# Kernel optimization log

Hardware: AMD Instinct MI355X
Metric: run time of the kernel (lower is better)

Reference implementation:

```python
import jax, jax.numpy as jnp
import numpy as np

N_NODES = 50000


def _sage_conv(x, src, dst, W_l, W_r, b, num_nodes):
    # message = x[src]; scatter-mean onto dst (PyG SAGEConv aggr='mean')
    msg = x[src]                                                # [E, C_in]
    agg_sum = jax.ops.segment_sum(msg, dst, num_segments=num_nodes)
    deg = jax.ops.segment_sum(jnp.ones((src.shape[0],), x.dtype), dst,
                              num_segments=num_nodes)
    agg = agg_sum / jnp.maximum(deg, 1.0)[:, None]              # mean, deg clamped to 1
    # lin_l(agg) + lin_r(x); bias lives in lin_l (PyG default)
    return agg @ W_l.T + x @ W_r.T + b


def setup_inputs() -> dict:
    key = jax.random.key(0)
    ks = jax.random.split(key, 8)
    C = 128
    s = 1.0 / np.sqrt(C)
    x = jax.random.normal(ks[0], (N_NODES, C), dtype=jnp.float32)
    edge_index = jax.random.randint(ks[1], (2, 800000), 0, N_NODES, dtype=jnp.int64)
    W1_l = jax.random.uniform(ks[2], (C, C), jnp.float32, -s, s)
    W1_r = jax.random.uniform(ks[3], (C, C), jnp.float32, -s, s)
    b1 = jax.random.uniform(ks[4], (C,), jnp.float32, -s, s)
    W2_l = jax.random.uniform(ks[5], (C, C), jnp.float32, -s, s)
    W2_r = jax.random.uniform(ks[6], (C, C), jnp.float32, -s, s)
    b2 = jax.random.uniform(ks[7], (C,), jnp.float32, -s, s)
    return {"x": x, "edge_index": edge_index,
            "W1_l": W1_l, "W1_r": W1_r, "b1": b1,
            "W2_l": W2_l, "W2_r": W2_r, "b2": b2}


def reference(x, edge_index, W1_l, W1_r, b1, W2_l, W2_r, b2):
    src, dst = edge_index[0], edge_index[1]
    h = _sage_conv(x, src, dst, W1_l, W1_r, b1, N_NODES)
    h = jax.nn.relu(h)  # dropout p=0.0 -> no-op
    out = _sage_conv(h, src, dst, W2_l, W2_r, b2, N_NODES)
    return out
```

## Files before the change

### kernel.cpp

```cpp
#include <hip/hip_runtime.h>

#define NCH 128
#define MAXBKT 512
#define BKT_SHIFT 7
#define BKT_NODES 128
#define BIN_BATCH 4096
#define NHIST 128

typedef __attribute__((ext_vector_type(8))) short bf16x8;
typedef __attribute__((ext_vector_type(4))) float f32x4;

__device__ __forceinline__ unsigned short f2bf_rne(float f) {
  unsigned u = __float_as_uint(f);
  unsigned r = u + 0x7FFF + ((u >> 16) & 1);
  return (unsigned short)(r >> 16);
}

__global__ __launch_bounds__(256) void k_bkthist(const int* __restrict__ dst,
                                                 int* __restrict__ partial,
                                                 int nE, int nBkt) {
  __shared__ int h[MAXBKT];
  int t = threadIdx.x;
  h[t] = 0; h[t + 256] = 0;
  __syncthreads();
  for (int e = blockIdx.x * 256 + t; e < nE; e += gridDim.x * 256)
    atomicAdd(&h[dst[e] >> BKT_SHIFT], 1);
  __syncthreads();
  partial[blockIdx.x * MAXBKT + t] = h[t];
  partial[blockIdx.x * MAXBKT + t + 256] = h[t + 256];
}

__global__ __launch_bounds__(512) void k_bktscan(const int* __restrict__ partial,
                                                 int* __restrict__ bktBase,
                                                 int* __restrict__ bktCursor, int nBkt) {
  __shared__ int sc[512];
  int t = threadIdx.x;
  int v = 0;
#pragma unroll 8
  for (int b = 0; b < NHIST; b++) v += partial[b * MAXBKT + t];
  sc[t] = v;
  __syncthreads();
  for (int off = 1; off < 512; off <<= 1) {
    int u = (t >= off) ? sc[t - off] : 0;
    __syncthreads();
    sc[t] += u;
    __syncthreads();
  }
  bktBase[t] = sc[t] - v;
  if (t == 511) bktBase[512] = sc[511];
  bktCursor[t] = 0;
}

__global__ __launch_bounds__(256) void k_bin(const int* __restrict__ src,
                                             const int* __restrict__ dst,
                                             const int* __restrict__ bktBase,
                                             int* __restrict__ bktCursor,
                                             uint2* __restrict__ binned,
                                             int nE, int nBkt) {
  __shared__ int hist[MAXBKT];
  __shared__ int boff[MAXBKT];
  int t = threadIdx.x;
  hist[t] = 0; hist[t + 256] = 0;
  __syncthreads();

  int eb = blockIdx.x * BIN_BATCH;
  uint2 pr[16];
  int rk[16];
#pragma unroll
  for (int i = 0; i < 16; i++) {
    int e = eb + t + i * 256;
    if (e < nE) {
      pr[i] = make_uint2((unsigned)src[e], (unsigned)dst[e]);
      rk[i] = atomicAdd(&hist[pr[i].y >> BKT_SHIFT], 1);
    } else rk[i] = -1;
  }
  __syncthreads();
  for (int i = t; i < nBkt; i += 256)
    boff[i] = hist[i] ? atomicAdd(&bktCursor[i], hist[i]) : 0;
  __syncthreads();
#pragma unroll
  for (int i = 0; i < 16; i++) {
    if (rk[i] >= 0) {
      int b = pr[i].y >> BKT_SHIFT;
      binned[bktBase[b] + boff[b] + rk[i]] = pr[i];
    }
  }
}

__global__ __launch_bounds__(256) void k_build(const uint2* __restrict__ binned,
                                               const int* __restrict__ bktBase,
                                               int* __restrict__ start,
                                               float* __restrict__ invdeg,
                                               int* __restrict__ srcSorted,
                                               int nN, int nE) {
  __shared__ int cnt[BKT_NODES];
  __shared__ int sc[BKT_NODES];
  __shared__ int cur[BKT_NODES];
  int b = blockIdx.x, t = threadIdx.x;
  int base = b << BKT_SHIFT;
  int e0 = bktBase[b], e1 = bktBase[b + 1];

  if (t < BKT_NODES) { cnt[t] = 0; cur[t] = 0; }
  __syncthreads();
  for (int i = e0 + t; i < e1; i += 256)
    atomicAdd(&cnt[binned[i].y - base], 1);
  __syncthreads();
  if (t < BKT_NODES) sc[t] = cnt[t];
  __syncthreads();
  for (int off = 1; off < BKT_NODES; off <<= 1) {
    int u = (t < BKT_NODES && t >= off) ? sc[t - off] : 0;
    __syncthreads();
    if (t < BKT_NODES && t >= off) sc[t] += u;
    __syncthreads();
  }
  if (t < BKT_NODES) {
    int n = base + t;
    if (n < nN) {
      start[n] = e0 + sc[t] - cnt[t];
      invdeg[n] = 1.0f / fmaxf((float)cnt[t], 1.0f);
    }
  }
  if (b == 0 && t == 0) start[nN] = nE;
  __syncthreads();
  for (int i = e0 + t; i < e1; i += 256) {
    uint2 p = binned[i];
    int ld = p.y - base;
    int pos = e0 + sc[ld] - cnt[ld] + atomicAdd(&cur[ld], 1);
    srcSorted[pos] = (int)p.x;
  }
}

__device__ __forceinline__ void prepW_elem(const float* __restrict__ Wl,
                                           const float* __restrict__ Wr,
                                           unsigned short* __restrict__ WhiF,
                                           unsigned short* __restrict__ WloF, int i) {
  int kc   = i >> 12;
  int r    = i & 4095;
  int nt   = r >> 9;
  int r2   = r & 511;
  int lane = r2 >> 3;
  int e    = r2 & 7;
  int j = nt * 16 + (lane & 15);
  int k = kc * 32 + (lane >> 4) * 8 + e;
  float w = (k < 128) ? Wl[j * 128 + k] : Wr[j * 128 + (k - 128)];
  unsigned u = __float_as_uint(w);
  float fhi = __uint_as_float(u & 0xFFFF0000u);
  float flo = w - fhi;
  WhiF[i] = (unsigned short)(u >> 16);
  WloF[i] = (unsigned short)(__float_as_uint(flo) >> 16);
}

__global__ __launch_bounds__(256) void k_prep(const float* __restrict__ x,
                                              unsigned short* __restrict__ xbf,
                                              const float* __restrict__ W1l,
                                              const float* __restrict__ W1r,
                                              const float* __restrict__ W2l,
                                              const float* __restrict__ W2r,
                                              unsigned short* __restrict__ W1hi,
                                              unsigned short* __restrict__ W1lo,
                                              unsigned short* __restrict__ W2hi,
                                              unsigned short* __restrict__ W2lo,
                                              int n8) {
  int i = blockIdx.x * 256 + threadIdx.x;
  if (i < n8) {
    const float4* p = reinterpret_cast<const float4*>(x + (size_t)i * 8);
    float4 v0 = p[0], v1 = p[1];
    uint4 o;
    o.x = (unsigned)f2bf_rne(v0.x) | ((unsigned)f2bf_rne(v0.y) << 16);
    o.y = (unsigned)f2bf_rne(v0.z) | ((unsigned)f2bf_rne(v0.w) << 16);
    o.z = (unsigned)f2bf_rne(v1.x) | ((unsigned)f2bf_rne(v1.y) << 16);
    o.w = (unsigned)f2bf_rne(v1.z) | ((unsigned)f2bf_rne(v1.w) << 16);
    *reinterpret_cast<uint4*>(xbf + (size_t)i * 8) = o;
  } else {
    int j = i - n8;
    if (j < 32768)       prepW_elem(W1l, W1r, W1hi, W1lo, j);
    else if (j < 65536)  prepW_elem(W2l, W2r, W2hi, W2lo, j - 32768);
  }
}

#define ACC8(v)                                          \
  a0 += __uint_as_float((v).x << 16);                    \
  a1 += __uint_as_float((v).x & 0xFFFF0000u);            \
  a2 += __uint_as_float((v).y << 16);                    \
  a3 += __uint_as_float((v).y & 0xFFFF0000u);            \
  a4 += __uint_as_float((v).z << 16);                    \
  a5 += __uint_as_float((v).z & 0xFFFF0000u);            \
  a6 += __uint_as_float((v).w << 16);                    \
  a7 += __uint_as_float((v).w & 0xFFFF0000u);

__global__ __launch_bounds__(256) void k_gather(const unsigned short* __restrict__ xbf,
                                                const int* __restrict__ srcSorted,
                                                const int* __restrict__ start,
                                                const float* __restrict__ invdeg,
                                                unsigned short* __restrict__ aggbf,
                                                int nN) {
  int gid = blockIdx.x * 256 + threadIdx.x;
  int node = gid >> 4;
  if (node >= nN) return;
  int c = (gid & 15) << 3;
  const unsigned short* xb = xbf + c;
  int s0 = start[node], s1 = start[node + 1];
  float a0 = 0.f, a1 = 0.f, a2 = 0.f, a3 = 0.f,
        a4 = 0.f, a5 = 0.f, a6 = 0.f, a7 = 0.f;
  int i = s0;
  for (; i + 4 <= s1; i += 4) {
    int sa = srcSorted[i],      sb = srcSorted[i + 1];
    int sc_ = srcSorted[i + 2], sd = srcSorted[i + 3];
    uint4 va = *reinterpret_cast<const uint4*>(xb + (size_t)sa * NCH);
    uint4 vb = *reinterpret_cast<const uint4*>(xb + (size_t)sb * NCH);
    uint4 vc = *reinterpret_cast<const uint4*>(xb + (size_t)sc_ * NCH);
    uint4 vd = *reinterpret_cast<const uint4*>(xb + (size_t)sd * NCH);
    ACC8(va) ACC8(vb) ACC8(vc) ACC8(vd)
  }
  for (; i < s1; i++) {
    int s = srcSorted[i];
    uint4 v = *reinterpret_cast<const uint4*>(xb + (size_t)s * NCH);
    ACC8(v)
  }
  float idg = invdeg[node];
  uint4 o;
  o.x = (unsigned)f2bf_rne(a0 * idg) | ((unsigned)f2bf_rne(a1 * idg) << 16);
  o.y = (unsigned)f2bf_rne(a2 * idg) | ((unsigned)f2bf_rne(a3 * idg) << 16);
  o.z = (unsigned)f2bf_rne(a4 * idg) | ((unsigned)f2bf_rne(a5 * idg) << 16);
  o.w = (unsigned)f2bf_rne(a6 * idg) | ((unsigned)f2bf_rne(a7 * idg) << 16);
  *reinterpret_cast<uint4*>(aggbf + (size_t)node * NCH + c) = o;
}

__global__ __launch_bounds__(256, 4) void k_linear_mfma(
    const unsigned short* __restrict__ aggbf, const unsigned short* __restrict__ xinbf,
    const unsigned short* __restrict__ Whi, const unsigned short* __restrict__ Wlo,
    const float* __restrict__ bias, float* __restrict__ outF,
    unsigned short* __restrict__ outBf, int relu, int nNodes) {
  int t = threadIdx.x;
  int wave = t >> 6;
  int lane = t & 63;
  int l15 = lane & 15;
  int lq  = lane >> 4;
  int r0 = (blockIdx.x * 4 + wave) * 16;

  const bf16x8* WhiV = reinterpret_cast<const bf16x8*>(Whi) + lane;
  const bf16x8* WloV = reinterpret_cast<const bf16x8*>(Wlo) + lane;

  f32x4 acc[8];
#pragma unroll
  for (int i = 0; i < 8; i++) acc[i] = (f32x4){0.f, 0.f, 0.f, 0.f};

  int arow = r0 + l15;
  if (arow >= nNodes) arow = nNodes - 1;

#pragma unroll
  for (int kc = 0; kc < 8; kc++) {
    const unsigned short* ab = (kc < 4) ? aggbf : xinbf;
    int k128 = (kc & 3) * 32 + lq * 8;
    bf16x8 a = *reinterpret_cast<const bf16x8*>(ab + (size_t)arow * NCH + k128);
#pragma unroll
    for (int nt = 0; nt < 8; nt++) {
      int fidx = (kc * 8 + nt) * 64;
      bf16x8 bhi = WhiV[fidx];
      bf16x8 blo = WloV[fidx];
      acc[nt] = __builtin_amdgcn_mfma_f32_16x16x32_bf16(a, bhi, acc[nt], 0, 0, 0);
      acc[nt] = __builtin_amdgcn_mfma_f32_16x16x32_bf16(a, blo, acc[nt], 0, 0, 0);
    }
  }

#pragma unroll
  for (int nt = 0; nt < 8; nt++) {
    int col = nt * 16 + l15;
    float bv = bias[col];
#pragma unroll
    for (int i = 0; i < 4; i++) {
      int row = r0 + lq * 4 + i;
      if (row < nNodes) {
        float v = acc[nt][i] + bv;
        if (relu) v = fmaxf(v, 0.f);
        if (outBf) outBf[(size_t)row * NCH + col] = f2bf_rne(v);
        else       outF[(size_t)row * NCH + col] = v;
      }
    }
  }
}

extern "C" void kernel_launch(void* const* d_in, const int* in_sizes, int n_in,
                              void* d_out, int out_size, void* d_ws, size_t ws_size,
                              hipStream_t stream) {
  const float* x   = (const float*)d_in[0];
  const int*   ei  = (const int*)d_in[1];
  const float* W1l = (const float*)d_in[2];
  const float* W1r = (const float*)d_in[3];
  const float* b1  = (const float*)d_in[4];
  const float* W2l = (const float*)d_in[5];
  const float* W2r = (const float*)d_in[6];
  const float* b2  = (const float*)d_in[7];
  float* out = (float*)d_out;

  const int nE = in_sizes[1] / 2;
  const int nN = in_sizes[0] / NCH;
  const int* src = ei;
  const int* dst = ei + nE;
  const int nBkt = (nN + BKT_NODES - 1) >> BKT_SHIFT;

  size_t bfBytes = (size_t)nN * NCH * sizeof(unsigned short);
  size_t wBytes  = (size_t)128 * 256 * sizeof(unsigned short);
  auto align256 = [](size_t v) { return (v + 255) & ~(size_t)255; };

  char* ws = (char*)d_ws;
  unsigned short* xbf   = (unsigned short*)ws;  ws += bfBytes;
  unsigned short* aggbf = (unsigned short*)ws;  ws += bfBytes;
  unsigned short* hbf   = (unsigned short*)ws;  ws += bfBytes;
  uint2* binned    = (uint2*)ws;                ws += (size_t)nE * sizeof(uint2);
  int*   srcSorted = (int*)ws;                  ws += align256((size_t)nE * sizeof(int));
  int*   startRow  = (int*)ws;                  ws += align256((size_t)(nN + 1) * sizeof(int));
  float* invdeg    = (float*)ws;                ws += align256((size_t)nN * sizeof(float));
  int*   partial   = (int*)ws;                  ws += (size_t)NHIST * MAXBKT * sizeof(int);
  int*   bktCursor = (int*)ws;                  ws += MAXBKT * sizeof(int);
  int*   bktBase   = (int*)ws;                  ws += align256((MAXBKT + 1) * sizeof(int));
  unsigned short* W1hi = (unsigned short*)ws;   ws += wBytes;
  unsigned short* W1lo = (unsigned short*)ws;   ws += wBytes;
  unsigned short* W2hi = (unsigned short*)ws;   ws += wBytes;
  unsigned short* W2lo = (unsigned short*)ws;   ws += wBytes;

  k_bkthist<<<NHIST, 256, 0, stream>>>(dst, partial, nE, nBkt);
  k_bktscan<<<1, 512, 0, stream>>>(partial, bktBase, bktCursor, nBkt);
  k_bin<<<(nE + BIN_BATCH - 1) / BIN_BATCH, 256, 0, stream>>>(src, dst, bktBase,
                                                              bktCursor, binned, nE, nBkt);
  k_build<<<nBkt, 256, 0, stream>>>(binned, bktBase, startRow, invdeg, srcSorted, nN, nE);

  {
    int n8 = nN * NCH / 8;
    int total = n8 + 2 * 32768;
    k_prep<<<(total + 255) / 256, 256, 0, stream>>>(x, xbf, W1l, W1r, W2l, W2r,
                                                    W1hi, W1lo, W2hi, W2lo, n8);
  }

  int gatherBlocks = (nN * 16 + 255) / 256;
  int linBlocks = (nN + 63) / 64;

  k_gather<<<gatherBlocks, 256, 0, stream>>>(xbf, srcSorted, startRow, invdeg, aggbf, nN);
  k_linear_mfma<<<linBlocks, 256, 0, stream>>>(aggbf, xbf, W1hi, W1lo, b1,
                                               nullptr, hbf, 1, nN);

  k_gather<<<gatherBlocks, 256, 0, stream>>>(hbf, srcSorted, startRow, invdeg, aggbf, nN);
  k_linear_mfma<<<linBlocks, 256, 0, stream>>>(aggbf, hbf, W2hi, W2lo, b2,
                                               out, nullptr, 0, nN);
}
```

Before: 158.8 us.

## Fuse gather-mean with MFMA linear per node tile and pack binned edges

Merges the neighbor gather/mean kernel and the MFMA linear kernel into one per-layer kernel. Each 512-thread block aggregates 128 nodes into swizzled LDS and then runs the bf16 MFMA on that tile, so the aggregated bf16 buffer is never written to or read back from global memory. The binned edge records also shrink from 8 bytes to 4 by packing a 16-bit source index with the local destination, and the histogram block count is halved. The 16-bit source packing assumes node ids fit in 16 bits, but N is 50000, which fits. The fused kernel has fewer blocks (391) and uses 32KB of LDS per block, which may reduce overlap of the latency-bound gather.

```diff
diff --git a/kernel.cpp b/kernel.cpp
--- a/kernel.cpp
+++ b/kernel.cpp
@@ -5,7 +5,8 @@
 #define BKT_SHIFT 7
 #define BKT_NODES 128
 #define BIN_BATCH 4096
-#define NHIST 128
+#define NHIST 64
+#define TILE_NODES 128
 
 typedef __attribute__((ext_vector_type(8))) short bf16x8;
 typedef __attribute__((ext_vector_type(4))) float f32x4;
@@ -55,7 +56,7 @@
                                              const int* __restrict__ dst,
                                              const int* __restrict__ bktBase,
                                              int* __restrict__ bktCursor,
-                                             uint2* __restrict__ binned,
+                                             unsigned* __restrict__ binned,
                                              int nE, int nBkt) {
   __shared__ int hist[MAXBKT];
   __shared__ int boff[MAXBKT];
@@ -64,14 +65,17 @@
   __syncthreads();
 
   int eb = blockIdx.x * BIN_BATCH;
-  uint2 pr[16];
+  unsigned pk[16];
+  short bkt[16];
   int rk[16];
 #pragma unroll
   for (int i = 0; i < 16; i++) {
     int e = eb + t + i * 256;
     if (e < nE) {
-      pr[i] = make_uint2((unsigned)src[e], (unsigned)dst[e]);
-      rk[i] = atomicAdd(&hist[pr[i].y >> BKT_SHIFT], 1);
+      int s = src[e], d = dst[e];
+      bkt[i] = (short)(d >> BKT_SHIFT);
+      pk[i] = (unsigned)s | ((unsigned)(d & (BKT_NODES - 1)) << 16);
+      rk[i] = atomicAdd(&hist[d >> BKT_SHIFT], 1);
     } else rk[i] = -1;
   }
   __syncthreads();
@@ -81,13 +85,13 @@
 #pragma unroll
   for (int i = 0; i < 16; i++) {
     if (rk[i] >= 0) {
-      int b = pr[i].y >> BKT_SHIFT;
-      binned[bktBase[b] + boff[b] + rk[i]] = pr[i];
-    }
-  }
-}
-
-__global__ __launch_bounds__(256) void k_build(const uint2* __restrict__ binned,
+      int b = bkt[i];
+      binned[bktBase[b] + boff[b] + rk[i]] = pk[i];
+    }
+  }
+}
+
+__global__ __launch_bounds__(256) void k_build(const unsigned* __restrict__ binned,
                                                const int* __restrict__ bktBase,
                                                int* __restrict__ start,
                                                float* __restrict__ invdeg,
@@ -103,7 +107,7 @@
   if (t < BKT_NODES) { cnt[t] = 0; cur[t] = 0; }
   __syncthreads();
   for (int i = e0 + t; i < e1; i += 256)
-    atomicAdd(&cnt[binned[i].y - base], 1);
+    atomicAdd(&cnt[binned[i] >> 16], 1);
   __syncthreads();
   if (t < BKT_NODES) sc[t] = cnt[t];
   __syncthreads();
@@ -123,10 +127,10 @@
   if (b == 0 && t == 0) start[nN] = nE;
   __syncthreads();
   for (int i = e0 + t; i < e1; i += 256) {
-    uint2 p = binned[i];
-    int ld = p.y - base;
+    unsigned p = binned[i];
+    int ld = p >> 16;
     int pos = e0 + sc[ld] - cnt[ld] + atomicAdd(&cur[ld], 1);
-    srcSorted[pos] = (int)p.x;
+    srcSorted[pos] = (int)(p & 0xFFFFu);
   }
 }
 
@@ -188,93 +192,110 @@
   a6 += __uint_as_float((v).w << 16);                    \
   a7 += __uint_as_float((v).w & 0xFFFF0000u);
 
-__global__ __launch_bounds__(256) void k_gather(const unsigned short* __restrict__ xbf,
-                                                const int* __restrict__ srcSorted,
-                                                const int* __restrict__ start,
-                                                const float* __restrict__ invdeg,
-                                                unsigned short* __restrict__ aggbf,
-                                                int nN) {
-  int gid = blockIdx.x * 256 + threadIdx.x;
-  int node = gid >> 4;
-  if (node >= nN) return;
-  int c = (gid & 15) << 3;
-  const unsigned short* xb = xbf + c;
-  int s0 = start[node], s1 = start[node + 1];
-  float a0 = 0.f, a1 = 0.f, a2 = 0.f, a3 = 0.f,
-        a4 = 0.f, a5 = 0.f, a6 = 0.f, a7 = 0.f;
-  int i = s0;
-  for (; i + 4 <= s1; i += 4) {
-    int sa = srcSorted[i],      sb = srcSorted[i + 1];
-    int sc_ = srcSorted[i + 2], sd = srcSorted[i + 3];
-    uint4 va = *reinterpret_cast<const uint4*>(xb + (size_t)sa * NCH);
-    uint4 vb = *reinterpret_cast<const uint4*>(xb + (size_t)sb * NCH);
-    uint4 vc = *reinterpret_cast<const uint4*>(xb + (size_t)sc_ * NCH);
-    uint4 vd = *reinterpret_cast<const uint4*>(xb + (size_t)sd * NCH);
-    ACC8(va) ACC8(vb) ACC8(vc) ACC8(vd)
-  }
-  for (; i < s1; i++) {
-    int s = srcSorted[i];
-    uint4 v = *reinterpret_cast<const uint4*>(xb + (size_t)s * NCH);
-    ACC8(v)
-  }
-  float idg = invdeg[node];
-  uint4 o;
-  o.x = (unsigned)f2bf_rne(a0 * idg) | ((unsigned)f2bf_rne(a1 * idg) << 16);
-  o.y = (unsigned)f2bf_rne(a2 * idg) | ((unsigned)f2bf_rne(a3 * idg) << 16);
-  o.z = (unsigned)f2bf_rne(a4 * idg) | ((unsigned)f2bf_rne(a5 * idg) << 16);
-  o.w = (unsigned)f2bf_rne(a6 * idg) | ((unsigned)f2bf_rne(a7 * idg) << 16);
-  *reinterpret_cast<uint4*>(aggbf + (size_t)node * NCH + c) = o;
-}
-
-__global__ __launch_bounds__(256, 4) void k_linear_mfma(
-    const unsigned short* __restrict__ aggbf, const unsigned short* __restrict__ xinbf,
+__global__ __launch_bounds__(512, 4) void k_layer(
+    const unsigned short* __restrict__ feat,
+    const int* __restrict__ srcSorted,
+    const int* __restrict__ start,
+    const float* __restrict__ invdeg,
     const unsigned short* __restrict__ Whi, const unsigned short* __restrict__ Wlo,
-    const float* __restrict__ bias, float* __restrict__ outF,
-    unsigned short* __restrict__ outBf, int relu, int nNodes) {
+    const float* __restrict__ bias,
+    float* __restrict__ outF, unsigned short* __restrict__ outBf,
+    int relu, int nN) {
+  __shared__ char lds[TILE_NODES * 256];
   int t = threadIdx.x;
-  int wave = t >> 6;
-  int lane = t & 63;
-  int l15 = lane & 15;
-  int lq  = lane >> 4;
-  int r0 = (blockIdx.x * 4 + wave) * 16;
-
-  const bf16x8* WhiV = reinterpret_cast<const bf16x8*>(Whi) + lane;
-  const bf16x8* WloV = reinterpret_cast<const bf16x8*>(Wlo) + lane;
-
-  f32x4 acc[8];
-#pragma unroll
-  for (int i = 0; i < 8; i++) acc[i] = (f32x4){0.f, 0.f, 0.f, 0.f};
-
-  int arow = r0 + l15;
-  if (arow >= nNodes) arow = nNodes - 1;
-
-#pragma unroll
-  for (int kc = 0; kc < 8; kc++) {
-    const unsigned short* ab = (kc < 4) ? aggbf : xinbf;
-    int k128 = (kc & 3) * 32 + lq * 8;
-    bf16x8 a = *reinterpret_cast<const bf16x8*>(ab + (size_t)arow * NCH + k128);
+  int node0 = blockIdx.x * TILE_NODES;
+
+  {
+    int r = t >> 4;
+    int c = (t & 15) << 3;
+    const unsigned short* xb = feat + c;
+#pragma unroll
+    for (int it = 0; it < 4; it++, r += 32) {
+      int node = node0 + r;
+      uint4 o = make_uint4(0u, 0u, 0u, 0u);
+      if (node < nN) {
+        int s0 = start[node], s1 = start[node + 1];
+        float a0 = 0.f, a1 = 0.f, a2 = 0.f, a3 = 0.f,
+              a4 = 0.f, a5 = 0.f, a6 = 0.f, a7 = 0.f;
+        int i = s0;
+        for (; i + 4 <= s1; i += 4) {
+          int sa = srcSorted[i],      sb = srcSorted[i + 1];
+          int sc_ = srcSorted[i + 2], sd = srcSorted[i + 3];
+          uint4 va = *reinterpret_cast<const uint4*>(xb + (size_t)sa * NCH);
+          uint4 vb = *reinterpret_cast<const uint4*>(xb + (size_t)sb * NCH);
+          uint4 vc = *reinterpret_cast<const uint4*>(xb + (size_t)sc_ * NCH);
+          uint4 vd = *reinterpret_cast<const uint4*>(xb + (size_t)sd * NCH);
+          ACC8(va) ACC8(vb) ACC8(vc) ACC8(vd)
+        }
+        for (; i < s1; i++) {
+          int s = srcSorted[i];
+          uint4 v = *reinterpret_cast<const uint4*>(xb + (size_t)s * NCH);
+          ACC8(v)
+        }
+        float idg = invdeg[node];
+        o.x = (unsigned)f2bf_rne(a0 * idg) | ((unsigned)f2bf_rne(a1 * idg) << 16);
+        o.y = (unsigned)f2bf_rne(a2 * idg) | ((unsigned)f2bf_rne(a3 * idg) << 16);
+        o.z = (unsigned)f2bf_rne(a4 * idg) | ((unsigned)f2bf_rne(a5 * idg) << 16);
+        o.w = (unsigned)f2bf_rne(a6 * idg) | ((unsigned)f2bf_rne(a7 * idg) << 16);
+      }
+      int cb = c * 2;
+      *reinterpret_cast<uint4*>(lds + r * 256 + (cb ^ ((r & 7) << 4))) = o;
+    }
+  }
+  __syncthreads();
+
+  {
+    int wave = t >> 6;
+    int lane = t & 63;
+    int l15 = lane & 15;
+    int lq  = lane >> 4;
+    int rloc0 = wave * 16;
+    int r0 = node0 + rloc0;
+
+    const bf16x8* WhiV = reinterpret_cast<const bf16x8*>(Whi) + lane;
+    const bf16x8* WloV = reinterpret_cast<const bf16x8*>(Wlo) + lane;
+
+    f32x4 acc[8];
+#pragma unroll
+    for (int i = 0; i < 8; i++) acc[i] = (f32x4){0.f, 0.f, 0.f, 0.f};
+
+    int arow = r0 + l15;
+    if (arow >= nN) arow = nN - 1;
+    int rloc = rloc0 + l15;
+
+#pragma unroll
+    for (int kc = 0; kc < 8; kc++) {
+      bf16x8 a;
+      if (kc < 4) {
+        int cb = ((kc & 3) * 32 + lq * 8) * 2;
+        a = *reinterpret_cast<const bf16x8*>(lds + rloc * 256 + (cb ^ ((rloc & 7) << 4)));
+      } else {
+        int k128 = (kc & 3) * 32 + lq * 8;
+        a = *reinterpret_cast<const bf16x8*>(feat + (size_t)arow * NCH + k128);
+      }
+#pragma unroll
+      for (int nt = 0; nt < 8; nt++) {
+        int fidx = (kc * 8 + nt) * 64;
+        bf16x8 bhi = WhiV[fidx];
+        bf16x8 blo = WloV[fidx];
+        acc[nt] = __builtin_amdgcn_mfma_f32_16x16x32_bf16(a, bhi, acc[nt], 0, 0, 0);
+        acc[nt] = __builtin_amdgcn_mfma_f32_16x16x32_bf16(a, blo, acc[nt], 0, 0, 0);
+      }
+    }
+
 #pragma unroll
     for (int nt = 0; nt < 8; nt++) {
-      int fidx = (kc * 8 + nt) * 64;
-      bf16x8 bhi = WhiV[fidx];
-      bf16x8 blo = WloV[fidx];
-      acc[nt] = __builtin_amdgcn_mfma_f32_16x16x32_bf16(a, bhi, acc[nt], 0, 0, 0);
-      acc[nt] = __builtin_amdgcn_mfma_f32_16x16x32_bf16(a, blo, acc[nt], 0, 0, 0);
-    }
-  }
-
-#pragma unroll
-  for (int nt = 0; nt < 8; nt++) {
-    int col = nt * 16 + l15;
-    float bv = bias[col];
-#pragma unroll
-    for (int i = 0; i < 4; i++) {
-      int row = r0 + lq * 4 + i;
-      if (row < nNodes) {
-        float v = acc[nt][i] + bv;
-        if (relu) v = fmaxf(v, 0.f);
-        if (outBf) outBf[(size_t)row * NCH + col] = f2bf_rne(v);
-        else       outF[(size_t)row * NCH + col] = v;
+      int col = nt * 16 + l15;
+      float bv = bias[col];
+#pragma unroll
+      for (int i = 0; i < 4; i++) {
+        int row = r0 + lq * 4 + i;
+        if (row < nN) {
+          float v = acc[nt][i] + bv;
+          if (relu) v = fmaxf(v, 0.f);
+          if (outBf) outBf[(size_t)row * NCH + col] = f2bf_rne(v);
+          else       outF[(size_t)row * NCH + col] = v;
+        }
       }
     }
   }
@@ -304,10 +325,9 @@
   auto align256 = [](size_t v) { return (v + 255) & ~(size_t)255; };
 
   char* ws = (char*)d_ws;
-  unsigned short* xbf   = (unsigned short*)ws;  ws += bfBytes;
-  unsigned short* aggbf = (unsigned short*)ws;  ws += bfBytes;
-  unsigned short* hbf   = (unsigned short*)ws;  ws += bfBytes;
-  uint2* binned    = (uint2*)ws;                ws += (size_t)nE * sizeof(uint2);
+  unsigned short* xbf = (unsigned short*)ws;    ws += bfBytes;
+  unsigned short* hbf = (unsigned short*)ws;    ws += bfBytes;
+  unsigned* binned = (unsigned*)ws;             ws += align256((size_t)nE * sizeof(unsigned));
   int*   srcSorted = (int*)ws;                  ws += align256((size_t)nE * sizeof(int));
   int*   startRow  = (int*)ws;                  ws += align256((size_t)(nN + 1) * sizeof(int));
   float* invdeg    = (float*)ws;                ws += align256((size_t)nN * sizeof(float));
@@ -332,14 +352,11 @@
                                                     W1hi, W1lo, W2hi, W2lo, n8);
   }
 
-  int gatherBlocks = (nN * 16 + 255) / 256;
-  int linBlocks = (nN + 63) / 64;
-
-  k_gather<<<gatherBlocks, 256, 0, stream>>>(xbf, srcSorted, startRow, invdeg, aggbf, nN);
-  k_linear_mfma<<<linBlocks, 256, 0, stream>>>(aggbf, xbf, W1hi, W1lo, b1,
-                                               nullptr, hbf, 1, nN);
-
-  k_gather<<<gatherBlocks, 256, 0, stream>>>(hbf, srcSorted, startRow, invdeg, aggbf, nN);
-  k_linear_mfma<<<linBlocks, 256, 0, stream>>>(aggbf, hbf, W2hi, W2lo, b2,
-                                               out, nullptr, 0, nN);
-}
+  int layerBlocks = (nN + TILE_NODES - 1) / TILE_NODES;
+
+  k_layer<<<layerBlocks, 512, 0, stream>>>(xbf, srcSorted, startRow, invdeg,
+                                           W1hi, W1lo, b1, nullptr, hbf, 1, nN);
+
+  k_layer<<<layerBlocks, 512, 0, stream>>>(hbf, srcSorted, startRow, invdeg,
+                                           W2hi, W2lo, b2, out, nullptr, 0, nN);
+}
```

After: 163.3 us. +2.9%, slower.
